# Optimization experiments

Measured on AMD Instinct MI355X. Metric: run time of the kernel, lower is better.

## Reference

```python
import jax, jax.numpy as jnp
import numpy as np

N = 8192
D_IN, D_GAT, D_GCN = 128, 64, 64


def setup_inputs() -> dict:
    key = jax.random.key(0)
    ks = jax.random.split(key, 7)
    feat = jax.random.normal(ks[0], (N, D_IN), dtype=jnp.float32)
    r = jax.random.uniform(ks[1], (N, N), dtype=jnp.float32)
    sup = jnp.where(r < 0.01, r * 100.0, 0.0)
    xav = lambda k, shape: jax.random.normal(k, shape, dtype=jnp.float32) * jnp.sqrt(2.0 / (shape[0] + shape[1]))
    W_map = xav(ks[2], (D_IN, D_GAT))
    b_map = jnp.zeros((1,), dtype=jnp.float32)
    U = xav(ks[3], (D_GAT, 1))
    V = xav(ks[4], (D_GAT, 1))
    W_gcn = xav(ks[5], (D_GAT, D_GCN))
    return {"feat": feat, "sup": sup, "W_map": W_map, "b_map": b_map, "U": U, "V": V, "W_gcn": W_gcn}


def reference(feat, sup, W_map, b_map, U, V, W_gcn):
    n = sup.shape[0]
    sup2 = sup + jnp.eye(n, dtype=sup.dtype)  # add self-loops
    # GAT layer
    h = feat @ W_map                            # [N, D_GAT]
    s = h @ U                                   # [N, 1] score from source node i
    t = h @ V                                   # [N, 1] score from target node j
    # torch loop builds att[j, i] = tanh(s_i + t_j + b)
    att = jnp.tanh(s.T + t + b_map)             # [N, N]
    att = jnp.where(sup2 > 0, att, jnp.float32(-100.0))
    att = jax.nn.softmax(att, axis=1)
    gat_feat = jnp.tanh(att @ h)                # [N, D_GAT]
    # GCN layer (dropout is identity at inference)
    agg = sup2 @ gat_feat                       # [N, D_GAT]
    out = jax.nn.relu(agg @ W_gcn)              # [N, D_GCN]
    norm = jnp.linalg.norm(out, axis=1, keepdims=True)
    out = out / jnp.maximum(norm, jnp.float32(1e-12))  # F.normalize(p=2, dim=1)
    return out
```

## Files before the change

### kernel.cpp

```cpp
#include <hip/hip_runtime.h>


#define N_NODES 8192
#define D_IN    128
#define D_GAT   64
#define SLOTS   256

#define COMPACT4(VX, QQ)                                                      \
    {                                                                         \
        float ee4[4] = {VX.x, VX.y, VX.z, VX.w};                              \
        _Pragma("unroll")                                                     \
        for (int u = 0; u < 4; ++u) {                                         \
            const int i = (QQ) * 4 + u;                                       \
            const float vv = ee4[u] + ((i == j) ? 1.0f : 0.0f);     \
            const bool keep = vv > 0.f;                                       \
            const unsigned long long mask = __ballot(keep);                   \
            if (keep) {                                                       \
                const int pos = base +                                        \
                    __popcll(mask & ((1ull << lane) - 1ull));                 \
                if (pos < SLOTS) { clr[pos] = i; vvr[pos] = vv; }             \
            }                                                                 \
            base += __popcll(mask);                                           \
        }                                                                     \
    }

#define GATHER32(SRC, WARR, CARR)                                             \
    {                                                                         \
        const int p0 = bse + pp,  p1 = p0 + 4,  p2 = p0 + 8,  p3 = p0 + 12;   \
        const int p4 = p0 + 16,   p5 = p0 + 20, p6 = p0 + 24, p7 = p0 + 28;   \
        const float e0 = WARR[p0], e1 = WARR[p1], e2 = WARR[p2], e3 = WARR[p3];\
        const float e4 = WARR[p4], e5 = WARR[p5], e6 = WARR[p6], e7 = WARR[p7];\
        const float4 v0 = *(const float4*)(SRC + CARR[p0] * D_GAT + c16);     \
        const float4 v1 = *(const float4*)(SRC + CARR[p1] * D_GAT + c16);     \
        const float4 v2 = *(const float4*)(SRC + CARR[p2] * D_GAT + c16);     \
        const float4 v3 = *(const float4*)(SRC + CARR[p3] * D_GAT + c16);     \
        const float4 v4 = *(const float4*)(SRC + CARR[p4] * D_GAT + c16);     \
        const float4 v5 = *(const float4*)(SRC + CARR[p5] * D_GAT + c16);     \
        const float4 v6 = *(const float4*)(SRC + CARR[p6] * D_GAT + c16);     \
        const float4 v7 = *(const float4*)(SRC + CARR[p7] * D_GAT + c16);     \
        a0.x += e0*v0.x; a0.y += e0*v0.y; a0.z += e0*v0.z; a0.w += e0*v0.w;   \
        a1.x += e1*v1.x; a1.y += e1*v1.y; a1.z += e1*v1.z; a1.w += e1*v1.w;   \
        a2.x += e2*v2.x; a2.y += e2*v2.y; a2.z += e2*v2.z; a2.w += e2*v2.w;   \
        a3.x += e3*v3.x; a3.y += e3*v3.y; a3.z += e3*v3.z; a3.w += e3*v3.w;   \
        a0.x += e4*v4.x; a0.y += e4*v4.y; a0.z += e4*v4.z; a0.w += e4*v4.w;   \
        a1.x += e5*v5.x; a1.y += e5*v5.y; a1.z += e5*v5.z; a1.w += e5*v5.w;   \
        a2.x += e6*v6.x; a2.y += e6*v6.y; a2.z += e6*v6.z; a2.w += e6*v6.w;   \
        a3.x += e7*v7.x; a3.y += e7*v7.y; a3.z += e7*v7.z; a3.w += e7*v7.w;   \
    }

__global__ __launch_bounds__(256) void k1_map(
    const float* __restrict__ feat, const float* __restrict__ W_map,
    const float* __restrict__ U, const float* __restrict__ V,
    float* __restrict__ h, float* __restrict__ s, float* __restrict__ t)
{
    const int wid  = threadIdx.x >> 6;
    const int lane = threadIdx.x & 63;
    const int row = blockIdx.x * 4 + wid;
    __shared__ float f[4 * D_IN];
    if (threadIdx.x < 128)
        ((float4*)f)[threadIdx.x] =
            ((const float4*)(feat + (size_t)blockIdx.x * 4 * D_IN))[threadIdx.x];
    __syncthreads();
    const float* fr = f + wid * D_IN;
    float acc = 0.f;
#pragma unroll 8
    for (int k = 0; k < D_IN; ++k)
        acc += fr[k] * W_map[k * D_GAT + lane];
    h[row * D_GAT + lane] = acc;
    float sv = acc * U[lane];
    float tv = acc * V[lane];
#pragma unroll
    for (int off = 32; off > 0; off >>= 1) {
        sv += __shfl_xor(sv, off);
        tv += __shfl_xor(tv, off);
    }
    if (lane == 0) { s[row] = sv; t[row] = tv; }
}

__global__ __launch_bounds__(256) void k23_compact_gat(
    const float* __restrict__ sup, const float* __restrict__ h,
    const float* __restrict__ s, const float* __restrict__ t,
    const float* __restrict__ b,
    int* __restrict__ cnt, int* __restrict__ col, float* __restrict__ val,
    float* __restrict__ gat)
{
    const int wid  = threadIdx.x >> 6;
    const int lane = threadIdx.x & 63;
    const int j = blockIdx.x * 4 + wid;

    __shared__ int   cl_s[4][SLOTS];
    __shared__ float vv_s[4][SLOTS];
    __shared__ float w_s[4][SLOTS];
    int*   clr = cl_s[wid];
    float* vvr = vv_s[wid];
    float* w   = w_s[wid];

    const float4* row4 = (const float4*)(sup + (size_t)j * N_NODES);
    int base = 0;
    for (int q = lane; q < N_NODES / 4; q += 256) {
        float4 v0 = row4[q];
        float4 v1 = row4[q + 64];
        float4 v2 = row4[q + 128];
        float4 v3 = row4[q + 192];
        COMPACT4(v0, q);
        COMPACT4(v1, q + 64);
        COMPACT4(v2, q + 128);
        COMPACT4(v3, q + 192);
    }
    const int m     = (base < SLOTS) ? base : SLOTS;
    const int m_pad = (m + 31) & ~31;
    __syncthreads();

    int*   colj = col + j * SLOTS;
    float* valj = val + j * SLOTS;
    const float tj = t[j] + b[0];
    float lsum = 0.f;
    for (int p = lane; p < m_pad; p += 64) {
        if (p < m) {
            const int ci = clr[p];
            colj[p] = ci;
            valj[p] = vvr[p];
            const float e = __expf(tanhf(s[ci] + tj));
            w[p] = e;
            lsum += e;
        } else {
            clr[p] = 0; w[p] = 0.f;
            colj[p] = 0; valj[p] = 0.f;
        }
    }
    if (lane == 0) cnt[j] = m_pad;
#pragma unroll
    for (int off = 32; off > 0; off >>= 1) lsum += __shfl_xor(lsum, off);
    __syncthreads();

    const int c16 = (lane & 15) * 4;
    const int pp  = lane >> 4;
    float4 a0 = make_float4(0,0,0,0), a1 = a0, a2 = a0, a3 = a0;
    for (int bse = 0; bse < m_pad; bse += 32)
        GATHER32(h, w, clr);
    float4 acc;
    acc.x = (a0.x + a1.x) + (a2.x + a3.x);
    acc.y = (a0.y + a1.y) + (a2.y + a3.y);
    acc.z = (a0.z + a1.z) + (a2.z + a3.z);
    acc.w = (a0.w + a1.w) + (a2.w + a3.w);
#pragma unroll
    for (int off = 16; off <= 32; off <<= 1) {
        acc.x += __shfl_xor(acc.x, off); acc.y += __shfl_xor(acc.y, off);
        acc.z += __shfl_xor(acc.z, off); acc.w += __shfl_xor(acc.w, off);
    }
    if (pp == 0) {
        const float inv = 1.0f / lsum;
        float4 o;
        o.x = tanhf(acc.x * inv); o.y = tanhf(acc.y * inv);
        o.z = tanhf(acc.z * inv); o.w = tanhf(acc.w * inv);
        *(float4*)(gat + j * D_GAT + c16) = o;
    }
}

__global__ __launch_bounds__(256) void k4_gcn(
    const float* __restrict__ gat, const float* __restrict__ W_gcn,
    const int* __restrict__ cnt, const int* __restrict__ col,
    const float* __restrict__ val, float* __restrict__ out)
{
    const int wid  = threadIdx.x >> 6;
    const int lane = threadIdx.x & 63;
    const int j = blockIdx.x * 4 + wid;
    const int m = cnt[j];
    const int*   colj = col + j * SLOTS;
    const float* valj = val + j * SLOTS;
    __shared__ int   cl_s[4][SLOTS];
    __shared__ float wv_s[4][SLOTS];
    __shared__ float a_s[4][D_GAT];
    int*   cl = cl_s[wid];
    float* wv = wv_s[wid];
    float* a  = a_s[wid];
    for (int p = lane; p < m; p += 64) { cl[p] = colj[p]; wv[p] = valj[p]; }
    __syncthreads();

    const int c16 = (lane & 15) * 4;
    const int pp  = lane >> 4;
    float4 a0 = make_float4(0,0,0,0), a1 = a0, a2 = a0, a3 = a0;
    for (int bse = 0; bse < m; bse += 32)
        GATHER32(gat, wv, cl);
    float4 acc;
    acc.x = (a0.x + a1.x) + (a2.x + a3.x);
    acc.y = (a0.y + a1.y) + (a2.y + a3.y);
    acc.z = (a0.z + a1.z) + (a2.z + a3.z);
    acc.w = (a0.w + a1.w) + (a2.w + a3.w);
#pragma unroll
    for (int off = 16; off <= 32; off <<= 1) {
        acc.x += __shfl_xor(acc.x, off); acc.y += __shfl_xor(acc.y, off);
        acc.z += __shfl_xor(acc.z, off); acc.w += __shfl_xor(acc.w, off);
    }
    if (pp == 0) *(float4*)(a + c16) = acc;
    __syncthreads();

    float o = 0.f;
#pragma unroll 8
    for (int d = 0; d < D_GAT; ++d)
        o += a[d] * W_gcn[d * D_GAT + lane];
    o = fmaxf(o, 0.f);

    float ss = o * o;
#pragma unroll
    for (int off = 32; off > 0; off >>= 1) ss += __shfl_xor(ss, off);
    const float nrm = sqrtf(ss);
    out[j * D_GAT + lane] = o / fmaxf(nrm, 1e-12f);
}

extern "C" void kernel_launch(void* const* d_in, const int* in_sizes, int n_in,
                              void* d_out, int out_size, void* d_ws, size_t ws_size,
                              hipStream_t stream) {
    const float* feat  = (const float*)d_in[0];
    const float* sup   = (const float*)d_in[1];
    const float* W_map = (const float*)d_in[2];
    const float* b_map = (const float*)d_in[3];
    const float* U     = (const float*)d_in[4];
    const float* V     = (const float*)d_in[5];
    const float* W_gcn = (const float*)d_in[6];
    float* out = (float*)d_out;

    char* ws = (char*)d_ws;
    float* h   = (float*)(ws);
    float* gat = (float*)(ws + (2u << 20));
    float* s   = (float*)(ws + (4u << 20));
    float* t   = (float*)(ws + (4u << 20) + 32768);
    int*   cnt = (int*)  (ws + (4u << 20) + 65536);
    int*   col = (int*)  (ws + (4u << 20) + 98304);
    float* val = (float*)(ws + (12u << 20) + 98304);

    k1_map<<<N_NODES / 4, 256, 0, stream>>>(feat, W_map, U, V, h, s, t);
    k23_compact_gat<<<N_NODES / 4, 256, 0, stream>>>(
        sup, h, s, t, b_map, cnt, col, val, gat);
    k4_gcn<<<N_NODES / 4, 256, 0, stream>>>(gat, W_gcn, cnt, col, val, out);
}
```

Measured before the change: 400.5 us.

## Apply W_gcn before GCN aggregation and pack column/value pairs into float2

Uses associativity (sup2 @ gat) @ W = sup2 @ (gat @ W) to move the dense W_gcn projection into the GAT kernel, so the GCN kernel only aggregates pre-projected rows and then applies ReLU and L2 normalisation. The dense product now runs once per node before aggregation rather than after it. The column indices and values of the compacted adjacency are stored interleaved as float2, so each is read with one load instead of two arrays. This changes the floating-point summation order slightly. The main cost, streaming the 256 MB adjacency in the compaction kernel, is unchanged.

New measurement: 400.2 us. No clear change (-0.1%).

```diff
diff --git a/kernel.cpp b/kernel.cpp
--- a/kernel.cpp
+++ b/kernel.cpp
@@ -80,9 +80,9 @@
 __global__ __launch_bounds__(256) void k23_compact_gat(
     const float* __restrict__ sup, const float* __restrict__ h,
     const float* __restrict__ s, const float* __restrict__ t,
-    const float* __restrict__ b,
-    int* __restrict__ cnt, int* __restrict__ col, float* __restrict__ val,
-    float* __restrict__ gat)
+    const float* __restrict__ b, const float* __restrict__ W_gcn,
+    int* __restrict__ cnt, float2* __restrict__ colval,
+    float* __restrict__ g2)
 {
     const int wid  = threadIdx.x >> 6;
     const int lane = threadIdx.x & 63;
@@ -111,21 +111,19 @@
     const int m_pad = (m + 31) & ~31;
     __syncthreads();
 
-    int*   colj = col + j * SLOTS;
-    float* valj = val + j * SLOTS;
+    float2* cvj = colval + j * SLOTS;
     const float tj = t[j] + b[0];
     float lsum = 0.f;
     for (int p = lane; p < m_pad; p += 64) {
         if (p < m) {
             const int ci = clr[p];
-            colj[p] = ci;
-            valj[p] = vvr[p];
+            cvj[p] = make_float2(__int_as_float(ci), vvr[p]);
             const float e = __expf(tanhf(s[ci] + tj));
             w[p] = e;
             lsum += e;
         } else {
             clr[p] = 0; w[p] = 0.f;
-            colj[p] = 0; valj[p] = 0.f;
+            cvj[p] = make_float2(__int_as_float(0), 0.f);
         }
     }
     if (lane == 0) cnt[j] = m_pad;
@@ -148,40 +146,45 @@
         acc.x += __shfl_xor(acc.x, off); acc.y += __shfl_xor(acc.y, off);
         acc.z += __shfl_xor(acc.z, off); acc.w += __shfl_xor(acc.w, off);
     }
-    if (pp == 0) {
-        const float inv = 1.0f / lsum;
-        float4 o;
-        o.x = tanhf(acc.x * inv); o.y = tanhf(acc.y * inv);
-        o.z = tanhf(acc.z * inv); o.w = tanhf(acc.w * inv);
-        *(float4*)(gat + j * D_GAT + c16) = o;
-    }
+    const float inv = 1.0f / lsum;
+    float4 gr;
+    gr.x = tanhf(acc.x * inv); gr.y = tanhf(acc.y * inv);
+    gr.z = tanhf(acc.z * inv); gr.w = tanhf(acc.w * inv);
+
+    if (pp == 0) *(float4*)(vvr + c16) = gr;
+    __syncthreads();
+    float o = 0.f;
+#pragma unroll 8
+    for (int k = 0; k < D_GAT; ++k)
+        o += vvr[k] * W_gcn[k * D_GAT + lane];
+    g2[j * D_GAT + lane] = o;
 }
 
 __global__ __launch_bounds__(256) void k4_gcn(
-    const float* __restrict__ gat, const float* __restrict__ W_gcn,
-    const int* __restrict__ cnt, const int* __restrict__ col,
-    const float* __restrict__ val, float* __restrict__ out)
+    const float* __restrict__ g2, const int* __restrict__ cnt,
+    const float2* __restrict__ colval, float* __restrict__ out)
 {
     const int wid  = threadIdx.x >> 6;
     const int lane = threadIdx.x & 63;
     const int j = blockIdx.x * 4 + wid;
     const int m = cnt[j];
-    const int*   colj = col + j * SLOTS;
-    const float* valj = val + j * SLOTS;
+    const float2* cvj = colval + j * SLOTS;
     __shared__ int   cl_s[4][SLOTS];
     __shared__ float wv_s[4][SLOTS];
-    __shared__ float a_s[4][D_GAT];
     int*   cl = cl_s[wid];
     float* wv = wv_s[wid];
-    float* a  = a_s[wid];
-    for (int p = lane; p < m; p += 64) { cl[p] = colj[p]; wv[p] = valj[p]; }
+    for (int p = lane; p < m; p += 64) {
+        const float2 cv = cvj[p];
+        cl[p] = __float_as_int(cv.x);
+        wv[p] = cv.y;
+    }
     __syncthreads();
 
     const int c16 = (lane & 15) * 4;
     const int pp  = lane >> 4;
     float4 a0 = make_float4(0,0,0,0), a1 = a0, a2 = a0, a3 = a0;
     for (int bse = 0; bse < m; bse += 32)
-        GATHER32(gat, wv, cl);
+        GATHER32(g2, wv, cl);
     float4 acc;
     acc.x = (a0.x + a1.x) + (a2.x + a3.x);
     acc.y = (a0.y + a1.y) + (a2.y + a3.y);
@@ -192,20 +195,19 @@
         acc.x += __shfl_xor(acc.x, off); acc.y += __shfl_xor(acc.y, off);
         acc.z += __shfl_xor(acc.z, off); acc.w += __shfl_xor(acc.w, off);
     }
-    if (pp == 0) *(float4*)(a + c16) = acc;
-    __syncthreads();
-
-    float o = 0.f;
-#pragma unroll 8
-    for (int d = 0; d < D_GAT; ++d)
-        o += a[d] * W_gcn[d * D_GAT + lane];
-    o = fmaxf(o, 0.f);
-
-    float ss = o * o;
-#pragma unroll
-    for (int off = 32; off > 0; off >>= 1) ss += __shfl_xor(ss, off);
-    const float nrm = sqrtf(ss);
-    out[j * D_GAT + lane] = o / fmaxf(nrm, 1e-12f);
+    float4 o4;
+    o4.x = fmaxf(acc.x, 0.f); o4.y = fmaxf(acc.y, 0.f);
+    o4.z = fmaxf(acc.z, 0.f); o4.w = fmaxf(acc.w, 0.f);
+    float ss = (o4.x*o4.x + o4.y*o4.y) + (o4.z*o4.z + o4.w*o4.w);
+#pragma unroll
+    for (int off = 1; off <= 8; off <<= 1) ss += __shfl_xor(ss, off);
+    const float inv = 1.0f / fmaxf(sqrtf(ss), 1e-12f);
+    if (pp == 0) {
+        float4 o;
+        o.x = o4.x * inv; o.y = o4.y * inv;
+        o.z = o4.z * inv; o.w = o4.w * inv;
+        *(float4*)(out + j * D_GAT + c16) = o;
+    }
 }
 
 extern "C" void kernel_launch(void* const* d_in, const int* in_sizes, int n_in,
@@ -221,16 +223,15 @@
     float* out = (float*)d_out;
 
     char* ws = (char*)d_ws;
-    float* h   = (float*)(ws);
-    float* gat = (float*)(ws + (2u << 20));
-    float* s   = (float*)(ws + (4u << 20));
-    float* t   = (float*)(ws + (4u << 20) + 32768);
-    int*   cnt = (int*)  (ws + (4u << 20) + 65536);
-    int*   col = (int*)  (ws + (4u << 20) + 98304);
-    float* val = (float*)(ws + (12u << 20) + 98304);
+    float*  h      = (float*)(ws);
+    float*  g2     = (float*)(ws + (2u << 20));
+    float*  s      = (float*)(ws + (4u << 20));
+    float*  t      = (float*)(ws + (4u << 20) + 32768);
+    int*    cnt    = (int*)  (ws + (4u << 20) + 65536);
+    float2* colval = (float2*)(ws + (4u << 20) + 98304);
 
     k1_map<<<N_NODES / 4, 256, 0, stream>>>(feat, W_map, U, V, h, s, t);
     k23_compact_gat<<<N_NODES / 4, 256, 0, stream>>>(
-        sup, h, s, t, b_map, cnt, col, val, gat);
-    k4_gcn<<<N_NODES / 4, 256, 0, stream>>>(gat, W_gcn, cnt, col, val, out);
-}
+        sup, h, s, t, b_map, W_gcn, cnt, colval, g2);
+    k4_gcn<<<N_NODES / 4, 256, 0, stream>>>(g2, cnt, colval, out);
+}
```
